# Kernel tuning notes

Measured on AMD Instinct MI355X. Metric: run time of the kernel, lower is better.

Reference implementation:

```python
import jax, jax.numpy as jnp
import numpy as np

N_NODES = 20000
N_EDGES = 320000
MUL = 64            # multiplicity of 0e and 1o node irreps
N_SPECIES = 5
N_BESSEL = 8
RAD_HIDDEN = 64
N_TP_W = 4 * MUL    # 4 uvu paths, 64 weights each
AVG_NEIGH = 16.0
SQ3 = np.sqrt(3.0).astype(np.float32)


def setup_inputs() -> dict:
    key = jax.random.key(0)
    ks = jax.random.split(key, 16)
    inp = {
        'node_feats': jax.random.normal(ks[0], (N_NODES, 4 * MUL), jnp.float32),
        'node_attrs': jax.random.uniform(ks[1], (N_NODES, N_SPECIES), jnp.float32),
        'edge_sh': jax.random.normal(ks[2], (N_EDGES, 4), jnp.float32),
        'senders': jax.random.randint(ks[3], (N_EDGES,), 0, N_NODES),
        'receivers': jax.random.randint(ks[4], (N_EDGES,), 0, N_NODES),
        'edge_embedded': jax.random.normal(ks[5], (N_EDGES, N_BESSEL), jnp.float32),
        # Linear on node feats (per-irrep mixing): 64x0e->64x0e, 64x1o->64x1o
        'Wl0': jax.random.normal(ks[6], (MUL, MUL), jnp.float32),
        'Wl1': jax.random.normal(ks[7], (MUL, MUL), jnp.float32),
        # radial MLP: 8 -> 64 -> 64 -> 256, no bias, scalar_mlp_std = 4.0
        'Wm1': jax.random.normal(ks[8], (N_BESSEL, RAD_HIDDEN), jnp.float32) * 4.0,
        'Wm2': jax.random.normal(ks[9], (RAD_HIDDEN, RAD_HIDDEN), jnp.float32) * 4.0,
        'Wm3': jax.random.normal(ks[10], (RAD_HIDDEN, N_TP_W), jnp.float32) * 4.0,
        # output Linear: (128x0e + 128x1o after TP) -> h_out (128x0e + 64x1o)
        'W2s': jax.random.normal(ks[11], (2 * MUL, 2 * MUL), jnp.float32),
        'W2v': jax.random.normal(ks[12], (2 * MUL, MUL), jnp.float32),
        # residual FullyConnectedTensorProduct(node_feats, node_attrs) -> h_out
        'Wr_s': jax.random.normal(ks[13], (MUL, N_SPECIES, 2 * MUL), jnp.float32),
        'Wr_v': jax.random.normal(ks[14], (MUL, N_SPECIES, MUL), jnp.float32),
    }
    return inp


def reference(node_feats, node_attrs, edge_sh, senders, receivers, edge_embedded,
              Wl0, Wl1, Wm1, Wm2, Wm3, W2s, W2v, Wr_s, Wr_v):
    N = node_feats.shape[0]
    x0 = node_feats[:, :MUL]                       # [N, 64]   0e scalars
    x1 = node_feats[:, MUL:].reshape(N, MUL, 3)    # [N, 64, 3] 1o vectors

    # --- residual FullyConnectedTensorProduct(node_feats, node_attrs) -> h_out ---
    # node_attrs are 0e scalars: paths 0e x 0e -> 0e and 1o x 0e -> 1o.
    nr = 1.0 / np.sqrt(MUL * N_SPECIES).astype(np.float32)  # fan-in norm
    res_s = jnp.einsum('nu,ns,usv->nv', x0, node_attrs, Wr_s) * nr   # [N, 128]
    res_v = jnp.einsum('num,ns,usv->nvm', x1, node_attrs, Wr_v) * nr # [N, 64, 3]

    # --- Linear(node_feats.irreps) ---
    nl = 1.0 / np.sqrt(MUL).astype(np.float32)
    y0 = (x0 @ Wl0) * nl                                  # [N, 64]
    y1 = jnp.einsum('num,uv->nvm', x1, Wl1) * nl          # [N, 64, 3]

    # --- gather to edges ---
    e0 = y0[senders]          # [E, 64]
    e1 = y1[senders]          # [E, 64, 3]
    sh0 = edge_sh[:, 0]       # [E]
    sh1 = edge_sh[:, 1:4]     # [E, 3]

    # --- radial MLP producing per-edge TP weights ---
    h = jax.nn.swish(edge_embedded @ Wm1 / np.sqrt(N_BESSEL, dtype=np.float32))
    h = jax.nn.swish(h @ Wm2 / np.sqrt(RAD_HIDDEN, dtype=np.float32))
    w = h @ Wm3 / np.sqrt(RAD_HIDDEN, dtype=np.float32)   # [E, 256]
    w1, w2, w3, w4 = (w[:, :MUL], w[:, MUL:2*MUL], w[:, 2*MUL:3*MUL], w[:, 3*MUL:])

    # --- equivariant tensor product (uvu), 4 paths ---
    # 0e x 0e -> 0e ; 1o x 1o -> 0e (CG = delta/sqrt(3))
    tp_s = jnp.concatenate([
        w1 * e0 * sh0[:, None],
        w4 * jnp.einsum('eum,em->eu', e1, sh1) / SQ3,
    ], axis=1)  # [E, 128]
    # 0e x 1o -> 1o ; 1o x 0e -> 1o
    tp_v = jnp.concatenate([
        w2[:, :, None] * e0[:, :, None] * sh1[:, None, :],
        w3[:, :, None] * e1 * sh0[:, None, None],
    ], axis=1)  # [E, 128, 3]

    # --- scatter-sum aggregation over receivers ---
    agg_s = jax.ops.segment_sum(tp_s, receivers, num_segments=N) / AVG_NEIGH          # [N, 128]
    agg_v = jax.ops.segment_sum(tp_v.reshape(-1, 2 * MUL * 3), receivers,
                                num_segments=N).reshape(N, 2 * MUL, 3) / AVG_NEIGH    # [N, 128, 3]

    # --- Linear(h_out_irreps) ---
    n2 = 1.0 / np.sqrt(2 * MUL).astype(np.float32)
    z_s = (agg_s @ W2s) * n2                               # [N, 128] (64 scalars + 64 gates)
    z_v = jnp.einsum('num,uv->nvm', agg_v, W2v) * n2       # [N, 64, 3]

    # residual connection
    z_s = z_s + res_s
    z_v = z_v + res_v

    # --- gate: even_act = swish on scalars and gate scalars; gated 1o vectors ---
    out_s = jax.nn.swish(z_s[:, :MUL])                     # [N, 64]
    gates = jax.nn.swish(z_s[:, MUL:])                     # [N, 64]
    out_v = gates[:, :, None] * z_v                        # [N, 64, 3]

    return jnp.concatenate([out_s, out_v.reshape(N, MUL * 3)], axis=1)  # [N, 256]
```

## Files before the change

### kernel.cpp

```cpp
#include <hip/hip_runtime.h>
#include <hip/hip_fp16.h>


#define NN 20000
#define NE 320000

typedef _Float16 h2v __attribute__((ext_vector_type(2)));
typedef _Float16 f16x8 __attribute__((ext_vector_type(8)));
typedef float f32x4 __attribute__((ext_vector_type(4)));

__device__ __forceinline__ float swishf(float x) {
  float t = __expf(-fabsf(x));
  float r = 1.0f / (1.0f + t);
  float sig = (x >= 0.0f) ? r : t * r;
  return x * sig;
}

__device__ __forceinline__ unsigned pack2h(float a, float b) {
  __half2 h = __floats2half2_rn(a, b);
  return *reinterpret_cast<unsigned*>(&h);
}

__device__ __forceinline__ h2v u32h2(unsigned u) {
  union { unsigned u; h2v h; } x; x.u = u; return x.h;
}

__device__ __forceinline__ h2v packh2v(float a, float b) {
  h2v h; h.x = (_Float16)a; h.y = (_Float16)b; return h;
}

__device__ __forceinline__ f16x8 u4f16(uint4 u) {
  union { uint4 u; f16x8 h; } x; x.u = u; return x.h;
}

__device__ __forceinline__ void ld8(float d[8], const float* p) {
  float4 a0 = *(const float4*)p;
  float4 a1 = *(const float4*)(p + 4);
  d[0]=a0.x; d[1]=a0.y; d[2]=a0.z; d[3]=a0.w;
  d[4]=a1.x; d[5]=a1.y; d[6]=a1.z; d[7]=a1.w;
}

__device__ __forceinline__ void fma8v(float (&acc)[8], const float* p, float w) {
  float4 a0 = *(const float4*)p;
  float4 a1 = *(const float4*)(p + 4);
  acc[0] = fmaf(a0.x, w, acc[0]); acc[1] = fmaf(a0.y, w, acc[1]);
  acc[2] = fmaf(a0.z, w, acc[2]); acc[3] = fmaf(a0.w, w, acc[3]);
  acc[4] = fmaf(a1.x, w, acc[4]); acc[5] = fmaf(a1.y, w, acc[5]);
  acc[6] = fmaf(a1.z, w, acc[6]); acc[7] = fmaf(a1.w, w, acc[7]);
}

__global__ __launch_bounds__(256) void hist_kernel(const int* __restrict__ rcv,
                                                   int* __restrict__ counts) {
  int e = blockIdx.x * 256 + threadIdx.x;
  atomicAdd(&counts[rcv[e]], 1);
}

__global__ __launch_bounds__(1024) void scan_kernel(const int* __restrict__ counts,
                                                    int* __restrict__ offsets,
                                                    int* __restrict__ cursor) {
  __shared__ int part[1024];
  const int t = threadIdx.x;
  const int base = t * 20;
  int loc[20];
  int s = 0;
  #pragma unroll
  for (int j = 0; j < 20; ++j) {
    int idx = base + j;
    int c = (idx < NN) ? counts[idx] : 0;
    loc[j] = s;
    s += c;
  }
  part[t] = s;
  __syncthreads();
  for (int d = 1; d < 1024; d <<= 1) {
    int v = (t >= d) ? part[t - d] : 0;
    __syncthreads();
    part[t] += v;
    __syncthreads();
  }
  int excl = (t > 0) ? part[t - 1] : 0;
  #pragma unroll
  for (int j = 0; j < 20; ++j) {
    int idx = base + j;
    if (idx < NN) {
      int o = excl + loc[j];
      offsets[idx] = o;
      cursor[idx] = o;
    }
  }
  if (t == 1023) offsets[NN] = part[1023];
}

__global__ __launch_bounds__(256) void scatter_full(
    const int* __restrict__ rcv, const int* __restrict__ snd,
    const float* __restrict__ esh, int* __restrict__ cursor,
    int* __restrict__ csr_edge, int* __restrict__ snd_sorted,
    float* __restrict__ sh_sorted) {
  int e = blockIdx.x * 256 + threadIdx.x;
  int r = rcv[e];
  int pos = atomicAdd(&cursor[r], 1);
  csr_edge[pos] = e;
  snd_sorted[pos] = snd[e];
  float4 sh = *(const float4*)(esh + (size_t)e * 4);
  *(float4*)(sh_sorted + (size_t)pos * 4) = sh;
}

__global__ __launch_bounds__(256) void scatter_kernel(
    const int* __restrict__ rcv, int* __restrict__ cursor,
    int* __restrict__ csr_edge) {
  int e = blockIdx.x * 256 + threadIdx.x;
  int r = rcv[e];
  int pos = atomicAdd(&cursor[r], 1);
  csr_edge[pos] = e;
}

__global__ __launch_bounds__(256) void pack_weights(
    const float* __restrict__ Wm2, const float* __restrict__ Wm3,
    unsigned* __restrict__ Wm2P, unsigned* __restrict__ Wm3P) {
  int idx = blockIdx.x * 256 + threadIdx.x;
  if (idx < 2048) {
    int k2 = idx >> 6, v = idx & 63;
    Wm2P[idx] = pack2h(Wm2[(2 * k2) * 64 + v], Wm2[(2 * k2 + 1) * 64 + v]);
  } else if (idx < 10240) {
    int r = idx - 2048;
    int k2 = r >> 8, c = r & 255;
    Wm3P[r] = pack2h(Wm3[(2 * k2) * 256 + c], Wm3[(2 * k2 + 1) * 256 + c]);
  }
}

__global__ __launch_bounds__(256) void pack_node_B(
    const float* __restrict__ Wr_s, const float* __restrict__ W2s,
    const float* __restrict__ Wr_v, const float* __restrict__ W2v,
    unsigned* __restrict__ BsT, unsigned* __restrict__ BvT) {
  const float nr = 0.05590169943749474f;
  const float n2 = 0.08838834764831845f;
  int idx = blockIdx.x * 256 + threadIdx.x;
  if (idx < 28672) {
    int v = idx / 224, j = idx % 224;
    float a, b;
    if (j < 160) {
      int s = j >> 5, u0 = (j & 31) << 1;
      a = Wr_s[(u0 * 5 + s) * 128 + v] * nr;
      b = Wr_s[((u0 + 1) * 5 + s) * 128 + v] * nr;
    } else {
      int c0 = (j - 160) << 1;
      a = W2s[c0 * 128 + v] * n2;
      b = W2s[(c0 + 1) * 128 + v] * n2;
    }
    BsT[idx] = pack2h(a, b);
  } else if (idx < 43008) {
    int r = idx - 28672;
    int v = r / 224, j = r % 224;
    float a, b;
    if (j < 160) {
      int s = j >> 5, u0 = (j & 31) << 1;
      a = Wr_v[(u0 * 5 + s) * 64 + v] * nr;
      b = Wr_v[((u0 + 1) * 5 + s) * 64 + v] * nr;
    } else {
      int c0 = (j - 160) << 1;
      a = W2v[c0 * 64 + v] * n2;
      b = W2v[(c0 + 1) * 64 + v] * n2;
    }
    BvT[r] = pack2h(a, b);
  }
}

__global__ __launch_bounds__(256) void node_prep(
    const float* __restrict__ feats, const float* __restrict__ Wl0,
    const float* __restrict__ Wl1, float* __restrict__ y)
{
  __shared__ __align__(16) float sX[4 * 256];
  const int t = threadIdx.x;
  const int n0 = blockIdx.x * 4;
  #pragma unroll
  for (int nb = 0; nb < 4; ++nb)
    sX[nb * 256 + t] = feats[(size_t)(n0 + nb) * 256 + t];
  __syncthreads();

  float acc[4] = {0.f, 0.f, 0.f, 0.f};
  if (t < 64) {
    const int v = t;
    for (int u = 0; u < 64; ++u) {
      float w = Wl0[u * 64 + v];
      acc[0] = fmaf(sX[0 * 256 + u], w, acc[0]);
      acc[1] = fmaf(sX[1 * 256 + u], w, acc[1]);
      acc[2] = fmaf(sX[2 * 256 + u], w, acc[2]);
      acc[3] = fmaf(sX[3 * 256 + u], w, acc[3]);
    }
  } else {
    const int i = t - 64;
    const int v = i / 3;
    const int m = i - v * 3;
    for (int u = 0; u < 64; ++u) {
      float w = Wl1[u * 64 + v];
      int xi = 64 + u * 3 + m;
      acc[0] = fmaf(sX[0 * 256 + xi], w, acc[0]);
      acc[1] = fmaf(sX[1 * 256 + xi], w, acc[1]);
      acc[2] = fmaf(sX[2 * 256 + xi], w, acc[2]);
      acc[3] = fmaf(sX[3 * 256 + xi], w, acc[3]);
    }
  }
  #pragma unroll
  for (int nb = 0; nb < 4; ++nb)
    y[(size_t)(n0 + nb) * 256 + t] = acc[nb] * 0.125f;
}

__device__ __forceinline__ void wgemv(float (&wa)[64], const float* __restrict__ Wm3,
                                      const float* h2col, int p)
{
  #pragma unroll
  for (int v = 0; v < 64; ++v) wa[v] = 0.f;
  #pragma unroll 2
  for (int k = 0; k < 64; ++k) {
    float h2k = h2col[k * 256];
    const float* wrow = Wm3 + k * 256 + p * 64;
    #pragma unroll
    for (int v = 0; v < 64; ++v) wa[v] = fmaf(h2k, wrow[v], wa[v]);
  }
}

__global__ __launch_bounds__(256) void w_kernel(
    const int* __restrict__ csr_edge, const float* __restrict__ emb,
    const float* __restrict__ Wm1, const unsigned* __restrict__ Wm2P,
    const unsigned* __restrict__ Wm3P, __half* __restrict__ w_sorted)
{
  __shared__ unsigned sA[256 * 32];
  __shared__ unsigned sB[256 * 32];
  const int tid = threadIdx.x;
  const int i = blockIdx.x * 256 + tid;
  const int e = csr_edge[i];

  {
    const int r = tid;
    #pragma unroll
    for (int c = 0; c < 8; ++c) {
      uint4 v;
      v.x = Wm3P[(4 * c + 0) * 256 + r];
      v.y = Wm3P[(4 * c + 1) * 256 + r];
      v.z = Wm3P[(4 * c + 2) * 256 + r];
      v.w = Wm3P[(4 * c + 3) * 256 + r];
      *(uint4*)&sB[r * 32 + ((c ^ (r & 7)) << 2)] = v;
    }
  }

  float e8[8];
  ld8(e8, emb + (size_t)e * 8);
  float h2a[64];
  #pragma unroll
  for (int v = 0; v < 64; ++v) h2a[v] = 0.f;
  #pragma unroll 1
  for (int k2 = 0; k2 < 32; ++k2) {
    float a0 = 0.f, a1 = 0.f;
    #pragma unroll
    for (int j = 0; j < 8; ++j) {
      a0 = fmaf(e8[j], Wm1[j * 64 + 2 * k2], a0);
      a1 = fmaf(e8[j], Wm1[j * 64 + 2 * k2 + 1], a1);
    }
    h2v ph = packh2v(swishf(a0 * 0.35355339059327373f),
                     swishf(a1 * 0.35355339059327373f));
    const unsigned* wrow = Wm2P + k2 * 64;
    #pragma unroll
    for (int v = 0; v < 64; ++v)
      h2a[v] = __builtin_amdgcn_fdot2(ph, u32h2(wrow[v]), h2a[v], false);
  }
  {
    const int r = tid;
    #pragma unroll
    for (int c = 0; c < 8; ++c) {
      uint4 v;
      v.x = pack2h(swishf(h2a[8 * c + 0] * 0.125f), swishf(h2a[8 * c + 1] * 0.125f));
      v.y = pack2h(swishf(h2a[8 * c + 2] * 0.125f), swishf(h2a[8 * c + 3] * 0.125f));
      v.z = pack2h(swishf(h2a[8 * c + 4] * 0.125f), swishf(h2a[8 * c + 5] * 0.125f));
      v.w = pack2h(swishf(h2a[8 * c + 6] * 0.125f), swishf(h2a[8 * c + 7] * 0.125f));
      *(uint4*)&sA[r * 32 + ((c ^ (r & 7)) << 2)] = v;
    }
  }
  __syncthreads();

  const int l = tid & 63;
  const int wv = tid >> 6;
  const int lg = l >> 4;
  const int lm = l & 15;

  f16x8 afr[4][2];
  #pragma unroll
  for (int mt = 0; mt < 4; ++mt) {
    int row = wv * 64 + mt * 16 + lm;
    #pragma unroll
    for (int kh = 0; kh < 2; ++kh) {
      uint4 u = *(const uint4*)&sA[row * 32 + ((((kh << 2) + lg) ^ (row & 7)) << 2)];
      afr[mt][kh] = u4f16(u);
    }
  }

  const size_t ebase = ((size_t)blockIdx.x * 256 + (size_t)wv * 64) * 256;
  #pragma unroll 1
  for (int nt = 0; nt < 16; ++nt) {
    int brow = nt * 16 + lm;
    uint4 u0 = *(const uint4*)&sB[brow * 32 + ((lg ^ (brow & 7)) << 2)];
    uint4 u1 = *(const uint4*)&sB[brow * 32 + (((4 + lg) ^ (brow & 7)) << 2)];
    f16x8 b0 = u4f16(u0), b1 = u4f16(u1);
    #pragma unroll
    for (int mt = 0; mt < 4; ++mt) {
      f32x4 acc = {0.f, 0.f, 0.f, 0.f};
      acc = __builtin_amdgcn_mfma_f32_16x16x32_f16(afr[mt][0], b0, acc, 0, 0, 0);
      acc = __builtin_amdgcn_mfma_f32_16x16x32_f16(afr[mt][1], b1, acc, 0, 0, 0);
      size_t o = ebase + (size_t)(mt * 16 + lg * 4) * 256 + nt * 16 + lm;
      #pragma unroll
      for (int rr = 0; rr < 4; ++rr)
        w_sorted[o + (size_t)rr * 256] = __float2half(acc[rr]);
    }
  }
}

__global__ __launch_bounds__(256) void gather_tp(
    const float* __restrict__ y, const __half* __restrict__ w_sorted,
    const float* __restrict__ sh_sorted, const int* __restrict__ snd_sorted,
    const int* __restrict__ offsets, float* __restrict__ agg)
{
  const int l = threadIdx.x & 63;
  const int wv = threadIdx.x >> 6;
  const int n = blockIdx.x * 4 + wv;
  const int row0 = offsets[n];
  const int row1 = offsets[n + 1];

  float s0 = 0.f, s1 = 0.f;
  float v0x = 0.f, v0y = 0.f, v0z = 0.f;
  float v1x = 0.f, v1y = 0.f, v1z = 0.f;

  for (int i = row0; i < row1; ++i) {
    const int s = snd_sorted[i];
    const float4 sh = *(const float4*)(sh_sorted + (size_t)i * 4);
    const __half* wr = w_sorted + (size_t)i * 256;
    float w1 = __half2float(wr[l]);
    float w2 = __half2float(wr[64 + l]);
    float w3 = __half2float(wr[128 + l]);
    float w4 = __half2float(wr[192 + l]);
    const float* yr = y + (size_t)s * 256;
    float e0 = yr[l];
    float ex = yr[64 + 3 * l], ey = yr[65 + 3 * l], ez = yr[66 + 3 * l];

    s0 = fmaf(w1 * e0, sh.x, s0);
    s1 = fmaf(w4, fmaf(ex, sh.y, fmaf(ey, sh.z, ez * sh.w)), s1);
    float t2 = w2 * e0;
    v0x = fmaf(t2, sh.y, v0x); v0y = fmaf(t2, sh.z, v0y); v0z = fmaf(t2, sh.w, v0z);
    float t3 = w3 * sh.x;
    v1x = fmaf(t3, ex, v1x); v1y = fmaf(t3, ey, v1y); v1z = fmaf(t3, ez, v1z);
  }

  const float SCL = 0.0078125f;
  const float C4  = 0.125f / (16.0f * 1.7320508075688772f);
  float* ar = agg + (size_t)n * 512;
  ar[l]       = s0 * SCL;
  ar[64 + l]  = s1 * C4;
  ar[128 + 3 * l]     = v0x * SCL;
  ar[128 + 3 * l + 1] = v0y * SCL;
  ar[128 + 3 * l + 2] = v0z * SCL;
  ar[320 + 3 * l]     = v1x * SCL;
  ar[320 + 3 * l + 1] = v1y * SCL;
  ar[320 + 3 * l + 2] = v1z * SCL;
}

__global__ __launch_bounds__(256) void node_gemm(
    const float* __restrict__ feats, const float* __restrict__ attrs,
    const float* __restrict__ agg, const unsigned* __restrict__ BsT,
    const unsigned* __restrict__ BvT, float* __restrict__ zs,
    float* __restrict__ zv)
{
  __shared__ unsigned sAK[64 * 224];
  __shared__ float sX[16 * 257];
  __shared__ float sAt[16 * 5];
  const int t = threadIdx.x;
  const int n0 = blockIdx.x * 16;

  #pragma unroll
  for (int nb = 0; nb < 16; ++nb)
    sX[nb * 257 + t] = feats[(size_t)(n0 + nb) * 256 + t];
  if (t < 80) sAt[t] = attrs[(size_t)n0 * 5 + t];
  __syncthreads();

  {
    const int row = t >> 2;
    const int part = t & 3;
    const bool is_s = row < 16;
    int node, m = 0;
    if (is_s) node = row;
    else { int vi = row - 16; node = vi / 3; m = vi - node * 3; }
    const float* xrow = &sX[node * 257];
    const float* atr = &sAt[node * 5];
    const float* aggr = agg + (size_t)(n0 + node) * 512;
    unsigned* arow = &sAK[row * 224];
    #pragma unroll 8
    for (int jj = 0; jj < 56; ++jj) {
      const int j = part + 4 * jj;
      float v0, v1;
      if (jj < 40) {
        int s = j >> 5;
        int u0 = (j & 31) << 1;
        float a = atr[s];
        float x0 = is_s ? xrow[u0]     : xrow[64 + 3 * u0 + m];
        float x1 = is_s ? xrow[u0 + 1] : xrow[64 + 3 * u0 + 3 + m];
        v0 = x0 * a;
        v1 = x1 * a;
      } else {
        int c0 = (j - 160) << 1;
        if (is_s) { v0 = aggr[c0]; v1 = aggr[c0 + 1]; }
        else {
          v0 = aggr[128 + 3 * c0 + m];
          v1 = aggr[128 + 3 * c0 + 3 + m];
        }
      }
      int chs = (jj & ~7) | ((jj ^ row) & 7);
      arow[(chs << 2) + part] = pack2h(v0, v1);
    }
  }
  __syncthreads();

  const int l = t & 63;
  const int wv = t >> 6;
  const int lm = l & 15;
  const int lg = l >> 4;

  #pragma unroll 1
  for (int jj = 0; jj < 5; ++jj) {
    const int jd = wv + 4 * jj;
    int mtile, ntile;
    const unsigned* Bt;
    if (jd < 8) { mtile = 0; ntile = jd; Bt = BsT; }
    else { int q = jd - 8; mtile = 1 + (q >> 2); ntile = q & 3; Bt = BvT; }

    const int arow0 = mtile * 16 + lm;
    const unsigned* brow = Bt + (ntile * 16 + lm) * 224;
    f32x4 acc = {0.f, 0.f, 0.f, 0.f};
    #pragma unroll 2
    for (int ks = 0; ks < 14; ++ks) {
      int ch = ks * 4 + lg;
      int chs = (ch & ~7) | ((ch ^ arow0) & 7);
      uint4 ua = *(const uint4*)&sAK[arow0 * 224 + (chs << 2)];
      uint4 ub = *(const uint4*)&brow[ch << 2];
      acc = __builtin_amdgcn_mfma_f32_16x16x32_f16(u4f16(ua), u4f16(ub), acc, 0, 0, 0);
    }
    const int drow = mtile * 16 + lg * 4;
    if (jd < 8) {
      #pragma unroll
      for (int rr = 0; rr < 4; ++rr)
        zs[(size_t)(n0 + drow + rr) * 128 + ntile * 16 + lm] = acc[rr];
    } else {
      const int vi0 = drow - 16;
      #pragma unroll
      for (int rr = 0; rr < 4; ++rr)
        zv[((size_t)blockIdx.x * 48 + vi0 + rr) * 64 + ntile * 16 + lm] = acc[rr];
    }
  }
}

__global__ __launch_bounds__(256) void gate_kernel(
    const float* __restrict__ zs, const float* __restrict__ zv,
    float* __restrict__ out)
{
  const int n = blockIdx.x;
  const int t = threadIdx.x;
  float val;
  if (t < 64) {
    val = swishf(zs[(size_t)n * 128 + t]);
  } else {
    int i = t - 64;
    int u = i / 3;
    int m = i - u * 3;
    float gate = swishf(zs[(size_t)n * 128 + 64 + u]);
    val = gate * zv[((size_t)n * 3 + m) * 64 + u];
  }
  out[(size_t)n * 256 + t] = val;
}

__global__ __launch_bounds__(512, 2) void gather_fused(
    const float* __restrict__ y, const int* __restrict__ csr_edge,
    const int* __restrict__ snd, const float* __restrict__ esh,
    const float* __restrict__ emb, const float* __restrict__ Wm1,
    const float* __restrict__ Wm2, const float* __restrict__ Wm3,
    const int* __restrict__ offsets, float* __restrict__ agg)
{
  __shared__ __align__(16) float sW3[64 * 256];
  __shared__ __align__(16) float sH[8 * 4 * 64];
  const int t = threadIdx.x;

  #pragma unroll 4
  for (int i = 0; i < 32; ++i) {
    int idx = i * 512 + t;
    int k = idx >> 8;
    int c = idx & 255;
    float v = Wm3[idx];
    int kg = k >> 2, kk = k & 3;
    sW3[c * 64 + (((kg ^ (c & 15)) & 15) << 2) + kk] = v;
  }
  __syncthreads();

  const int l = t & 63;
  const int wv = t >> 6;
  const int n = blockIdx.x * 8 + wv;
  const int row0 = offsets[n];
  const int row1 = offsets[n + 1];

  float* sHw = &sH[wv * 256];

  float wm1r[8];
  #pragma unroll
  for (int j = 0; j < 8; ++j) wm1r[j] = Wm1[j * 64 + l];

  float s0 = 0.f, s1 = 0.f;
  float v0x = 0.f, v0y = 0.f, v0z = 0.f;
  float v1x = 0.f, v1y = 0.f, v1z = 0.f;

  const int swz = ((l & 15) << 2);

  for (int i = row0; i < row1; i += 4) {
    const int nb = row1 - i;

    int   sn[4];
    float4 sh[4];
    #pragma unroll
    for (int b = 0; b < 4; ++b) {
      int idx = (b < nb) ? (i + b) : i;
      int e = csr_edge[idx];
      sn[b] = snd[e];
      float4 s = *(const float4*)(esh + (size_t)e * 4);
      if (b >= nb) s = make_float4(0.f, 0.f, 0.f, 0.f);
      sh[b] = s;
      float em8[8];
      ld8(em8, emb + (size_t)e * 8);
      float a = 0.f;
      #pragma unroll
      for (int j = 0; j < 8; ++j) a = fmaf(em8[j], wm1r[j], a);
      sHw[b * 64 + l] = swishf(a * 0.35355339059327373f);
    }

    float h2[4] = {0.f, 0.f, 0.f, 0.f};
    #pragma unroll 4
    for (int q = 0; q < 16; ++q) {
      float wq0 = Wm2[(4 * q + 0) * 64 + l];
      float wq1 = Wm2[(4 * q + 1) * 64 + l];
      float wq2 = Wm2[(4 * q + 2) * 64 + l];
      float wq3 = Wm2[(4 * q + 3) * 64 + l];
      #pragma unroll
      for (int b = 0; b < 4; ++b) {
        float4 h = *(const float4*)&sHw[b * 64 + 4 * q];
        h2[b] = fmaf(h.x, wq0, h2[b]);
        h2[b] = fmaf(h.y, wq1, h2[b]);
        h2[b] = fmaf(h.z, wq2, h2[b]);
        h2[b] = fmaf(h.w, wq3, h2[b]);
      }
    }
    #pragma unroll
    for (int b = 0; b < 4; ++b)
      h2[b] = swishf(h2[b] * 0.125f);
    #pragma unroll
    for (int b = 0; b < 4; ++b)
      sHw[b * 64 + l] = h2[b];

    float w0[4]  = {0,0,0,0}, w1a[4] = {0,0,0,0};
    float w2a[4] = {0,0,0,0}, w3a[4] = {0,0,0,0};
    #pragma unroll 1
    for (int g = 0; g < 16; ++g) {
      int sbase = l * 64 + (((g << 2) ^ swz) & 63);
      float4 m0 = *(const float4*)&sW3[sbase];
      float4 m1 = *(const float4*)&sW3[sbase + 4096];
      float4 m2 = *(const float4*)&sW3[sbase + 8192];
      float4 m3 = *(const float4*)&sW3[sbase + 12288];
      #pragma unroll
      for (int b = 0; b < 4; ++b) {
        float4 hb = *(const float4*)&sHw[b * 64 + 4 * g];
        #pragma unroll
        for (int kk = 0; kk < 4; ++kk) {
          float bc = (&hb.x)[kk];
          w0[b]  = fmaf(bc, (&m0.x)[kk], w0[b]);
          w1a[b] = fmaf(bc, (&m1.x)[kk], w1a[b]);
          w2a[b] = fmaf(bc, (&m2.x)[kk], w2a[b]);
          w3a[b] = fmaf(bc, (&m3.x)[kk], w3a[b]);
        }
      }
    }

    #pragma unroll
    for (int b = 0; b < 4; ++b) {
      const float* yr = y + (size_t)sn[b] * 256;
      float e0 = yr[l];
      float ex = yr[64 + 3 * l], ey = yr[65 + 3 * l], ez = yr[66 + 3 * l];
      float4 s = sh[b];
      s0 = fmaf(w0[b] * e0, s.x, s0);
      s1 = fmaf(w3a[b], fmaf(ex, s.y, fmaf(ey, s.z, ez * s.w)), s1);
      float t2 = w1a[b] * e0;
      v0x = fmaf(t2, s.y, v0x); v0y = fmaf(t2, s.z, v0y); v0z = fmaf(t2, s.w, v0z);
      float t3 = w2a[b] * s.x;
      v1x = fmaf(t3, ex, v1x); v1y = fmaf(t3, ey, v1y); v1z = fmaf(t3, ez, v1z);
    }
  }

  const float SCL = 0.0078125f;
  const float C4  = 0.125f / (16.0f * 1.7320508075688772f);
  float* ar = agg + (size_t)n * 512;
  ar[l]       = s0 * SCL;
  ar[64 + l]  = s1 * C4;
  ar[128 + 3 * l]     = v0x * SCL;
  ar[128 + 3 * l + 1] = v0y * SCL;
  ar[128 + 3 * l + 2] = v0z * SCL;
  ar[320 + 3 * l]     = v1x * SCL;
  ar[320 + 3 * l + 1] = v1y * SCL;
  ar[320 + 3 * l + 2] = v1z * SCL;
}

__global__ __launch_bounds__(256) void edge_kernel(
    const float* __restrict__ y, const float* __restrict__ edge_sh,
    const int* __restrict__ senders, const int* __restrict__ receivers,
    const float* __restrict__ emb, const float* __restrict__ Wm1,
    const float* __restrict__ Wm2, const float* __restrict__ Wm3,
    float* __restrict__ agg)
{
  __shared__ float h2s[64 * 256];
  const int tid = threadIdx.x;
  const int e = blockIdx.x * 256 + tid;
  const int s = senders[e];
  const int r = receivers[e];
  const float4 shv = *(const float4*)(edge_sh + (size_t)e * 4);
  float e8[8];
  ld8(e8, emb + (size_t)e * 8);

  float h2a[64];
  #pragma unroll
  for (int v = 0; v < 64; ++v) h2a[v] = 0.f;
  #pragma unroll 2
  for (int k = 0; k < 64; ++k) {
    float a = 0.f;
    #pragma unroll
    for (int j = 0; j < 8; ++j) a = fmaf(e8[j], Wm1[j * 64 + k], a);
    float h1k = swishf(a * 0.35355339059327373f);
    const float* wrow = Wm2 + k * 64;
    #pragma unroll
    for (int v = 0; v < 64; ++v) h2a[v] = fmaf(h1k, wrow[v], h2a[v]);
  }
  #pragma unroll
  for (int v = 0; v < 64; ++v)
    h2s[v * 256 + tid] = swishf(h2a[v] * 0.125f);

  const float* yrow = y + (size_t)s * 256;
  float* aggr = agg + (size_t)r * 512;
  const float SCL = 0.0078125f;
  const float c0  = shv.x * SCL;
  const float c1x = shv.y * SCL, c1y = shv.z * SCL, c1z = shv.w * SCL;
  const float c4  = 0.125f / (16.0f * 1.7320508075688772f);

  float wa[64];

  wgemv(wa, Wm3, h2s + tid, 0);
  #pragma unroll
  for (int uc = 0; uc < 8; ++uc) {
    float ev[8];
    ld8(ev, yrow + uc * 8);
    #pragma unroll
    for (int j = 0; j < 8; ++j) {
      int u = uc * 8 + j;
      atomicAdd(&aggr[u], wa[u] * ev[j] * c0);
    }
  }
  wgemv(wa, Wm3, h2s + tid, 1);
  #pragma unroll
  for (int uc = 0; uc < 8; ++uc) {
    float ev[8];
    ld8(ev, yrow + uc * 8);
    #pragma unroll
    for (int j = 0; j < 8; ++j) {
      int u = uc * 8 + j;
      float tt = wa[u] * ev[j];
      atomicAdd(&aggr[128 + 3 * u    ], tt * c1x);
      atomicAdd(&aggr[128 + 3 * u + 1], tt * c1y);
      atomicAdd(&aggr[128 + 3 * u + 2], tt * c1z);
    }
  }
  wgemv(wa, Wm3, h2s + tid, 2);
  #pragma unroll
  for (int uc = 0; uc < 8; ++uc) {
    float ev[24];
    ld8(ev,      yrow + 64 + uc * 24);
    ld8(ev + 8,  yrow + 64 + uc * 24 + 8);
    ld8(ev + 16, yrow + 64 + uc * 24 + 16);
    #pragma unroll
    for (int j = 0; j < 8; ++j) {
      int u = uc * 8 + j;
      float tt = wa[u] * c0;
      atomicAdd(&aggr[320 + 3 * u    ], tt * ev[3 * j    ]);
      atomicAdd(&aggr[320 + 3 * u + 1], tt * ev[3 * j + 1]);
      atomicAdd(&aggr[320 + 3 * u + 2], tt * ev[3 * j + 2]);
    }
  }
  wgemv(wa, Wm3, h2s + tid, 3);
  #pragma unroll
  for (int uc = 0; uc < 8; ++uc) {
    float ev[24];
    ld8(ev,      yrow + 64 + uc * 24);
    ld8(ev + 8,  yrow + 64 + uc * 24 + 8);
    ld8(ev + 16, yrow + 64 + uc * 24 + 16);
    #pragma unroll
    for (int j = 0; j < 8; ++j) {
      int u = uc * 8 + j;
      float d = ev[3*j]*shv.y + ev[3*j+1]*shv.z + ev[3*j+2]*shv.w;
      atomicAdd(&aggr[64 + u], wa[u] * d * c4);
    }
  }
}

__global__ __launch_bounds__(256) void node_post(
    const float* __restrict__ feats, const float* __restrict__ attrs,
    const float* __restrict__ agg, const float* __restrict__ W2s,
    const float* __restrict__ W2v, const float* __restrict__ Wr_s,
    const float* __restrict__ Wr_v, float* __restrict__ out)
{
  __shared__ __align__(16) float sA[320 * 8];
  __shared__ __align__(16) float sX0[64 * 8];
  __shared__ __align__(16) float sX1[192 * 8];
  __shared__ __align__(16) float sAt[5 * 8];
  __shared__ __align__(16) float sAggS[128 * 8];
  __shared__ __align__(16) float sAggV[384 * 8];
  __shared__ __align__(16) float sZs[8 * 128];
  __shared__ __align__(16) float sZv[8 * 192];

  const int t = threadIdx.x;
  const int n0 = blockIdx.x * 8;
  const float nr = 0.05590169943749474f;
  const float n2 = 0.08838834764831845f;

  #pragma unroll
  for (int nb = 0; nb < 8; ++nb) {
    float v = feats[(size_t)(n0 + nb) * 256 + t];
    if (t < 64) sX0[t * 8 + nb] = v;
    else        sX1[(t - 64) * 8 + nb] = v;
  }
  if (t < 40) {
    int nb = t & 7, s = t >> 3;
    sAt[s * 8 + nb] = attrs[(size_t)(n0 + nb) * 5 + s] * nr;
  }
  #pragma unroll
  for (int i = 0; i < 16; ++i) {
    int idx = i * 256 + t;
    int nb = idx >> 9;
    int c = idx & 511;
    float v = agg[(size_t)(n0 + nb) * 512 + c] * n2;
    if (c < 128) sAggS[c * 8 + nb] = v;
    else         sAggV[(c - 128) * 8 + nb] = v;
  }
  __syncthreads();

  #pragma unroll
  for (int i = 0; i < 10; ++i) {
    int idx = i * 256 + t;
    int nb = idx & 7;
    int us = idx >> 3;
    int u = us / 5;
    int s = us - u * 5;
    sA[us * 8 + nb] = sX0[u * 8 + nb] * sAt[s * 8 + nb];
  }
  __syncthreads();

  float av[8][3];

  if (t < 128) {
    const int v = t;
    float acc[8];
    #pragma unroll
    for (int nb = 0; nb < 8; ++nb) acc[nb] = 0.f;
    for (int us = 0; us < 320; ++us)
      fma8v(acc, &sA[us * 8], Wr_s[us * 128 + v]);
    for (int c = 0; c < 128; ++c)
      fma8v(acc, &sAggS[c * 8], W2s[c * 128 + v]);
    #pragma unroll
    for (int nb = 0; nb < 8; ++nb) sZs[nb * 128 + v] = acc[nb];
  } else {
    const int tv = t - 128;
    const int v = tv & 63;
    const int half = tv >> 6;
    #pragma unroll
    for (int nb = 0; nb < 8; ++nb)
      #pragma unroll
      for (int m = 0; m < 3; ++m) av[nb][m] = 0.f;

    const int u0 = half * 32;
    for (int u = u0; u < u0 + 32; ++u) {
      float xr0[8], xr1[8], xr2[8];
      ld8(xr0, &sX1[(u * 3 + 0) * 8]);
      ld8(xr1, &sX1[(u * 3 + 1) * 8]);
      ld8(xr2, &sX1[(u * 3 + 2) * 8]);
      #pragma unroll
      for (int s = 0; s < 5; ++s) {
        float w = Wr_v[(u * 5 + s) * 64 + v];
        float at[8];
        ld8(at, &sAt[s * 8]);
        #pragma unroll
        for (int nb = 0; nb < 8; ++nb) {
          float tt = at[nb] * w;
          av[nb][0] = fmaf(xr0[nb], tt, av[nb][0]);
          av[nb][1] = fmaf(xr1[nb], tt, av[nb][1]);
          av[nb][2] = fmaf(xr2[nb], tt, av[nb][2]);
        }
      }
    }
    const int c0 = half * 64;
    for (int c = c0; c < c0 + 64; ++c) {
      float w = W2v[c * 64 + v];
      float g0[8], g1[8], g2[8];
      ld8(g0, &sAggV[(c * 3 + 0) * 8]);
      ld8(g1, &sAggV[(c * 3 + 1) * 8]);
      ld8(g2, &sAggV[(c * 3 + 2) * 8]);
      #pragma unroll
      for (int nb = 0; nb < 8; ++nb) {
        av[nb][0] = fmaf(g0[nb], w, av[nb][0]);
        av[nb][1] = fmaf(g1[nb], w, av[nb][1]);
        av[nb][2] = fmaf(g2[nb], w, av[nb][2]);
      }
    }
    if (half == 0) {
      #pragma unroll
      for (int nb = 0; nb < 8; ++nb)
        #pragma unroll
        for (int m = 0; m < 3; ++m)
          sZv[nb * 192 + v * 3 + m] = av[nb][m];
    }
  }
  __syncthreads();
  if (t >= 192) {
    const int v = (t - 128) & 63;
    #pragma unroll
    for (int nb = 0; nb < 8; ++nb)
      #pragma unroll
      for (int m = 0; m < 3; ++m)
        sZv[nb * 192 + v * 3 + m] += av[nb][m];
  }
  __syncthreads();

  const int i = t - 64;
  const int ug = (t >= 64) ? (i / 3) : 0;
  #pragma unroll
  for (int nb = 0; nb < 8; ++nb) {
    float val;
    if (t < 64) {
      val = swishf(sZs[nb * 128 + t]);
    } else {
      float gate = swishf(sZs[nb * 128 + 64 + ug]);
      val = gate * sZv[nb * 192 + i];
    }
    out[(size_t)(n0 + nb) * 256 + t] = val;
  }
}

extern "C" void kernel_launch(void* const* d_in, const int* in_sizes, int n_in,
                              void* d_out, int out_size, void* d_ws, size_t ws_size,
                              hipStream_t stream)
{
  const float* feats = (const float*)d_in[0];
  const float* attrs = (const float*)d_in[1];
  const float* esh   = (const float*)d_in[2];
  const int*   snd   = (const int*)d_in[3];
  const int*   rcv   = (const int*)d_in[4];
  const float* emb   = (const float*)d_in[5];
  const float* Wl0   = (const float*)d_in[6];
  const float* Wl1   = (const float*)d_in[7];
  const float* Wm1   = (const float*)d_in[8];
  const float* Wm2   = (const float*)d_in[9];
  const float* Wm3   = (const float*)d_in[10];
  const float* W2s   = (const float*)d_in[11];
  const float* W2v   = (const float*)d_in[12];
  const float* Wr_s  = (const float*)d_in[13];
  const float* Wr_v  = (const float*)d_in[14];
  float* out = (float*)d_out;

  float* y   = (float*)d_ws;
  float* agg = y + (size_t)NN * 256;
  int* counts = (int*)agg;
  int* cursor = counts + NN;
  int* csr_edge = (int*)(agg + (size_t)NN * 512);
  int* offsets  = csr_edge + NE;
  int* snd_sorted = offsets + NN + 1;
  float* sh_sorted = (float*)(snd_sorted + NE);
  __half* w_sorted = (__half*)(sh_sorted + (size_t)NE * 4);
  unsigned* Wm2P = (unsigned*)(w_sorted + (size_t)NE * 256);
  unsigned* Wm3P = Wm2P + 2048;
  unsigned* BsT  = Wm3P + 8192;
  unsigned* BvT  = BsT + 28672;
  float* zs = y;
  float* zv = (float*)w_sorted;
  size_t need1 = (size_t)((char*)(BvT + 14336) - (char*)d_ws);
  size_t need2 = (size_t)((char*)(offsets + NN + 1) - (char*)d_ws);

  if (ws_size >= need1) {
    hipMemsetAsync(counts, 0, (size_t)NN * sizeof(int), stream);
    hist_kernel<<<NE / 256, 256, 0, stream>>>(rcv, counts);
    scan_kernel<<<1, 1024, 0, stream>>>(counts, offsets, cursor);
    scatter_full<<<NE / 256, 256, 0, stream>>>(rcv, snd, esh, cursor,
                                               csr_edge, snd_sorted, sh_sorted);
    pack_weights<<<40, 256, 0, stream>>>(Wm2, Wm3, Wm2P, Wm3P);
    pack_node_B<<<168, 256, 0, stream>>>(Wr_s, W2s, Wr_v, W2v, BsT, BvT);
    node_prep<<<NN / 4, 256, 0, stream>>>(feats, Wl0, Wl1, y);
    w_kernel<<<NE / 256, 256, 0, stream>>>(csr_edge, emb, Wm1, Wm2P, Wm3P, w_sorted);
    gather_tp<<<NN / 4, 256, 0, stream>>>(y, w_sorted, sh_sorted, snd_sorted,
                                          offsets, agg);
    node_gemm<<<NN / 16, 256, 0, stream>>>(feats, attrs, agg, BsT, BvT, zs, zv);
    gate_kernel<<<NN, 256, 0, stream>>>(zs, zv, out);
  } else if (ws_size >= need2) {
    hipMemsetAsync(counts, 0, (size_t)NN * sizeof(int), stream);
    hist_kernel<<<NE / 256, 256, 0, stream>>>(rcv, counts);
    scan_kernel<<<1, 1024, 0, stream>>>(counts, offsets, cursor);
    scatter_kernel<<<NE / 256, 256, 0, stream>>>(rcv, cursor, csr_edge);
    node_prep<<<NN / 4, 256, 0, stream>>>(feats, Wl0, Wl1, y);
    gather_fused<<<NN / 8, 512, 0, stream>>>(y, csr_edge, snd, esh, emb,
                                             Wm1, Wm2, Wm3, offsets, agg);
    node_post<<<NN / 8, 256, 0, stream>>>(feats, attrs, agg, W2s, W2v, Wr_s, Wr_v, out);
  } else {
    hipMemsetAsync(agg, 0, (size_t)NN * 512 * sizeof(float), stream);
    node_prep<<<NN / 4, 256, 0, stream>>>(feats, Wl0, Wl1, y);
    edge_kernel<<<NE / 256, 256, 0, stream>>>(y, esh, snd, rcv, emb, Wm1, Wm2, Wm3, agg);
    node_post<<<NN / 8, 256, 0, stream>>>(feats, attrs, agg, W2s, W2v, Wr_s, Wr_v, out);
  }
}
```

Before: 372.6 us.

## Stage MFMA outputs through LDS and write per-path weight planes with 16-byte stores

The radial-MLP weight kernel now transposes each wave's MFMA tile through swizzled shared memory. It then writes 128-bit vectorized rows into four separate per-path planes, replacing the scattered 2-byte stores it used before. The gather kernel reads each path's weights from its plane at a stride of 64 halves per edge. The aim is coalesced, wide global writes for the 164 MB weight tensor. The cost is extra LDS traffic, and the sA buffer is reused, which assumes the A fragments are already in registers.

Result: slower. 390.9 us (+4.9%).

```diff
diff --git a/kernel.cpp b/kernel.cpp
--- a/kernel.cpp
+++ b/kernel.cpp
@@ -31,6 +31,11 @@
 
 __device__ __forceinline__ f16x8 u4f16(uint4 u) {
   union { uint4 u; f16x8 h; } x; x.u = u; return x.h;
+}
+
+__device__ __forceinline__ unsigned short f16bits(float x) {
+  __half h = __float2half(x);
+  return *reinterpret_cast<unsigned short*>(&h);
 }
 
 __device__ __forceinline__ void ld8(float d[8], const float* p) {
@@ -222,7 +227,7 @@
 __global__ __launch_bounds__(256) void w_kernel(
     const int* __restrict__ csr_edge, const float* __restrict__ emb,
     const float* __restrict__ Wm1, const unsigned* __restrict__ Wm2P,
-    const unsigned* __restrict__ Wm3P, __half* __restrict__ w_sorted)
+    const unsigned* __restrict__ Wm3P, __half* __restrict__ w_planes)
 {
   __shared__ unsigned sA[256 * 32];
   __shared__ unsigned sB[256 * 32];
@@ -293,28 +298,43 @@
     }
   }
 
-  const size_t ebase = ((size_t)blockIdx.x * 256 + (size_t)wv * 64) * 256;
+  unsigned short* sT = (unsigned short*)sA + wv * 4096;
+  const int eb = blockIdx.x * 256 + wv * 64;
+
   #pragma unroll 1
-  for (int nt = 0; nt < 16; ++nt) {
-    int brow = nt * 16 + lm;
-    uint4 u0 = *(const uint4*)&sB[brow * 32 + ((lg ^ (brow & 7)) << 2)];
-    uint4 u1 = *(const uint4*)&sB[brow * 32 + (((4 + lg) ^ (brow & 7)) << 2)];
-    f16x8 b0 = u4f16(u0), b1 = u4f16(u1);
-    #pragma unroll
-    for (int mt = 0; mt < 4; ++mt) {
-      f32x4 acc = {0.f, 0.f, 0.f, 0.f};
-      acc = __builtin_amdgcn_mfma_f32_16x16x32_f16(afr[mt][0], b0, acc, 0, 0, 0);
-      acc = __builtin_amdgcn_mfma_f32_16x16x32_f16(afr[mt][1], b1, acc, 0, 0, 0);
-      size_t o = ebase + (size_t)(mt * 16 + lg * 4) * 256 + nt * 16 + lm;
-      #pragma unroll
-      for (int rr = 0; rr < 4; ++rr)
-        w_sorted[o + (size_t)rr * 256] = __float2half(acc[rr]);
+  for (int p = 0; p < 4; ++p) {
+    #pragma unroll
+    for (int ntl = 0; ntl < 4; ++ntl) {
+      const int nt = p * 4 + ntl;
+      int brow = nt * 16 + lm;
+      uint4 u0 = *(const uint4*)&sB[brow * 32 + ((lg ^ (brow & 7)) << 2)];
+      uint4 u1 = *(const uint4*)&sB[brow * 32 + (((4 + lg) ^ (brow & 7)) << 2)];
+      f16x8 b0 = u4f16(u0), b1 = u4f16(u1);
+      const int ch0 = ntl * 2 + (lm >> 3);
+      const int cl = lm & 7;
+      #pragma unroll
+      for (int mt = 0; mt < 4; ++mt) {
+        f32x4 acc = {0.f, 0.f, 0.f, 0.f};
+        acc = __builtin_amdgcn_mfma_f32_16x16x32_f16(afr[mt][0], b0, acc, 0, 0, 0);
+        acc = __builtin_amdgcn_mfma_f32_16x16x32_f16(afr[mt][1], b1, acc, 0, 0, 0);
+        #pragma unroll
+        for (int rr = 0; rr < 4; ++rr) {
+          int er = mt * 16 + lg * 4 + rr;
+          sT[er * 64 + (((ch0 ^ (er & 7)) << 3) | cl)] = f16bits(acc[rr]);
+        }
+      }
+    }
+    __half* dst = w_planes + ((size_t)p * NE + eb + l) * 64;
+    #pragma unroll
+    for (int ch = 0; ch < 8; ++ch) {
+      uint4 v = *(const uint4*)&sT[l * 64 + ((ch ^ (l & 7)) << 3)];
+      *(uint4*)((unsigned short*)dst + ch * 8) = v;
     }
   }
 }
 
 __global__ __launch_bounds__(256) void gather_tp(
-    const float* __restrict__ y, const __half* __restrict__ w_sorted,
+    const float* __restrict__ y, const __half* __restrict__ w_planes,
     const float* __restrict__ sh_sorted, const int* __restrict__ snd_sorted,
     const int* __restrict__ offsets, float* __restrict__ agg)
 {
@@ -323,6 +343,7 @@
   const int n = blockIdx.x * 4 + wv;
   const int row0 = offsets[n];
   const int row1 = offsets[n + 1];
+  const size_t PL = (size_t)NE * 64;
 
   float s0 = 0.f, s1 = 0.f;
   float v0x = 0.f, v0y = 0.f, v0z = 0.f;
@@ -331,11 +352,11 @@
   for (int i = row0; i < row1; ++i) {
     const int s = snd_sorted[i];
     const float4 sh = *(const float4*)(sh_sorted + (size_t)i * 4);
-    const __half* wr = w_sorted + (size_t)i * 256;
-    float w1 = __half2float(wr[l]);
-    float w2 = __half2float(wr[64 + l]);
-    float w3 = __half2float(wr[128 + l]);
-    float w4 = __half2float(wr[192 + l]);
+    const __half* wr = w_planes + (size_t)i * 64 + l;
+    float w1 = __half2float(wr[0]);
+    float w2 = __half2float(wr[PL]);
+    float w3 = __half2float(wr[2 * PL]);
+    float w4 = __half2float(wr[3 * PL]);
     const float* yr = y + (size_t)s * 256;
     float e0 = yr[l];
     float ex = yr[64 + 3 * l], ey = yr[65 + 3 * l], ez = yr[66 + 3 * l];
```
